# Kernel tuning notes

Measured on AMD Instinct MI355X. Metric: run time of the kernel, lower is better.

## Reference

```python
import jax, jax.numpy as jnp
import numpy as np
import math

B, H, W, CIN = 8, 64, 64, 192
INNER, K, N, P = 384, 2, 32, 64
NHK = INNER // P          # heads per scan direction = 6
NH = K * NHK              # total heads = 12
HID = 4 * CIN

def _silu(v):
    return v * jax.nn.sigmoid(v)

def setup_inputs() -> dict:
    key = jax.random.key(0)
    ks = jax.random.split(key, 12)
    x = jax.random.normal(ks[0], (B, H, W, CIN), jnp.float32)
    W_in = jax.random.normal(ks[1], (2 * INNER, CIN), jnp.float32) * 0.02
    conv_w = jax.random.normal(ks[2], (INNER, 1, 3, 3), jnp.float32) * 0.1
    conv_b = jnp.zeros((INNER,), jnp.float32)
    x_proj_weight = jax.random.normal(ks[3], (K, 2 * N + NHK, INNER), jnp.float32) * 0.02
    A_logs = jnp.log(jax.random.uniform(ks[4], (NH,), jnp.float32, 1.0, 16.0))
    Ds = jnp.ones((NH,), jnp.float32)
    u = jax.random.uniform(ks[5], (NH,), jnp.float32)
    dt = jnp.exp(u * (math.log(0.1) - math.log(0.001)) + math.log(0.001))
    dt = jnp.clip(dt, 1e-4, None)
    dt_bias = dt + jnp.log(-jnp.expm1(-dt))
    init_states = jnp.zeros((NH, P, N), jnp.float32)
    W_out = jax.random.normal(ks[6], (CIN, INNER), jnp.float32) * 0.02
    W1 = jax.random.normal(ks[7], (HID, CIN), jnp.float32) * 0.02
    b1 = jnp.zeros((HID,), jnp.float32)
    W2 = jax.random.normal(ks[8], (CIN, HID), jnp.float32) * 0.02
    b2 = jnp.zeros((CIN,), jnp.float32)
    return dict(x=x, W_in=W_in, conv_w=conv_w, conv_b=conv_b, x_proj_weight=x_proj_weight,
                A_logs=A_logs, Ds=Ds, dt_bias=dt_bias, init_states=init_states,
                W_out=W_out, W1=W1, b1=b1, W2=W2, b2=b2)

def reference(x, W_in, conv_w, conv_b, x_proj_weight, A_logs, Ds, dt_bias,
              init_states, W_out, W1, b1, W2, b2):
    Bb, Hh, Ww, Cin = x.shape
    L = Hh * Ww
    inner = W_in.shape[0] // 2
    shortcut = x
    # norm1 is identity (norm=None). in_proj (no bias), split into x and gate z
    xz = jnp.einsum('bhwc,dc->bhwd', x, W_in)
    xl, z = jnp.split(xz, 2, axis=-1)
    # depthwise conv (NCHW) + SiLU
    xc = jnp.transpose(xl, (0, 3, 1, 2))
    xc = jax.lax.conv_general_dilated(xc, conv_w, (1, 1), 'SAME',
                                      feature_group_count=inner,
                                      dimension_numbers=('NCHW', 'OIHW', 'NCHW'))
    xc = _silu(xc + conv_b[None, :, None, None])
    # cross scan: row-major and transposed (W-major) flattenings
    xs = jnp.stack([xc.reshape(Bb, inner, L),
                    jnp.transpose(xc, (0, 1, 3, 2)).reshape(Bb, inner, L)], axis=1)  # (B,K,inner,L)
    # project to B, C, dt per direction
    BCdt = jnp.einsum('bkdl,kcd->blkc', xs, x_proj_weight)  # (B,L,K,2N+NHK)
    Bs = BCdt[..., :N]                     # (B,L,K,N)
    Cs = BCdt[..., N:2 * N]                # (B,L,K,N)
    dt = BCdt[..., 2 * N:].reshape(Bb, L, NH)
    xh = jnp.transpose(xs, (0, 3, 1, 2)).reshape(Bb, L, NH, P)  # heads: k-major
    # Mamba2 selective scan (dt_softplus with bias)
    dt = jax.nn.softplus(dt + dt_bias)     # (B,L,NH)
    A = -jnp.exp(A_logs)                   # (NH,)
    da = jnp.exp(dt * A)                   # (B,L,NH)
    dtx = dt[..., None] * xh               # (B,L,NH,P)
    Bh = jnp.repeat(Bs, NHK, axis=2)       # (B,L,NH,N) group -> heads
    Ch = jnp.repeat(Cs, NHK, axis=2)
    h0 = jnp.broadcast_to(init_states, (Bb,) + init_states.shape)  # (B,NH,P,N)
    def step(h, inp):
        da_t, dtx_t, B_t, C_t = inp
        h = da_t[..., None, None] * h + dtx_t[..., None] * B_t[:, :, None, :]
        y_t = jnp.einsum('bhpn,bhn->bhp', h, C_t)
        return h, y_t
    _, ys = jax.lax.scan(step, h0, (jnp.moveaxis(da, 1, 0), jnp.moveaxis(dtx, 1, 0),
                                    jnp.moveaxis(Bh, 1, 0), jnp.moveaxis(Ch, 1, 0)))
    y = jnp.moveaxis(ys, 0, 1) + Ds[None, None, :, None] * xh  # (B,L,NH,P)
    out_y = jnp.transpose(y.reshape(Bb, L, K, inner), (0, 2, 3, 1))  # (B,K,inner,L)
    # scan_proj: undo each direction's flattening and sum
    y0 = out_y[:, 0].reshape(Bb, inner, Hh, Ww)
    y1 = jnp.transpose(out_y[:, 1].reshape(Bb, inner, Ww, Hh), (0, 1, 3, 2))
    yr = jnp.transpose((y0 + y1).reshape(Bb, inner, L), (0, 2, 1)).reshape(Bb, Hh, Ww, inner)
    # gate, out_proj, residual, MLP branch (dense is identity since in==out)
    yg = yr * _silu(z)
    out = shortcut + jnp.einsum('bhwd,cd->bhwc', yg, W_out)
    h1 = _silu(jnp.einsum('...c,dc->...d', out, W1) + b1)
    mlp = jnp.einsum('...d,cd->...c', h1, W2) + b2
    return out + mlp
```

## Files before the change

kernel.cpp:

```cpp
#include <hip/hip_runtime.h>
#include <math.h>

#define BB 8
#define HH 64
#define WW 64
#define CIN 192
#define INNER 384
#define LL 4096
#define NSTATE 32
#define PDIM 64
#define NHK 6
#define NHEADS 12
#define HID 768
#define CPROJ 70
#define QC 64
#define NC 64

#define WS_XLZ   0u
#define WS_XC    50331648u
#define WS_Y1    75497472u
#define WS_BCBF  100663296u
#define WS_DTRAW 109051904u
#define WS_DTV   119013376u
#define WS_CUMS  120586240u
#define WS_SHB   122159104u
#define WS_Y0    147324928u
#define WS_WINB  185073664u
#define WS_WPADB 185368576u
#define WS_WOUTB 185565184u
#define WS_W1B   185761792u
#define WS_W2B   186056704u
#define WS_REQ   186449920u

typedef __attribute__((ext_vector_type(8))) short short8;
typedef __attribute__((ext_vector_type(4))) float f32x4;

__device__ __forceinline__ float silu_f(float x) { return x / (1.f + __expf(-x)); }

__device__ __forceinline__ unsigned short f2bf(float f) {
    unsigned u = __float_as_uint(f);
    u += 0x7fffu + ((u >> 16) & 1u);
    return (unsigned short)(u >> 16);
}
__device__ __forceinline__ float bf2f(unsigned short u) {
    return __uint_as_float(((unsigned)u) << 16);
}

template<int AMODE>
__device__ __forceinline__ short8 load_a(const void* A, const unsigned short* Ay0,
                                         const unsigned short* Ay1, const unsigned short* Az,
                                         int row, int col, int Kd)
{
    if constexpr (AMODE == 0) {
        return *(const short8*)((const unsigned short*)A + (size_t)row * Kd + col);
    } else if constexpr (AMODE == 1) {
        const float* Af = (const float*)A + (size_t)row * Kd + col;
        const float4 v0 = *(const float4*)(Af);
        const float4 v1 = *(const float4*)(Af + 4);
        short8 r;
        r[0]=(short)f2bf(v0.x); r[1]=(short)f2bf(v0.y); r[2]=(short)f2bf(v0.z); r[3]=(short)f2bf(v0.w);
        r[4]=(short)f2bf(v1.x); r[5]=(short)f2bf(v1.y); r[6]=(short)f2bf(v1.z); r[7]=(short)f2bf(v1.w);
        return r;
    } else {
        const size_t yo = (size_t)row * INNER + col;
        const uint4 a  = *(const uint4*)(Ay0 + yo);
        const uint4 bv = *(const uint4*)(Ay1 + yo);
        const uint4 zv = *(const uint4*)(Az + (size_t)row * 768 + INNER + col);
        const unsigned ua[4]={a.x,a.y,a.z,a.w}, ub[4]={bv.x,bv.y,bv.z,bv.w}, uz[4]={zv.x,zv.y,zv.z,zv.w};
        short8 r;
        #pragma unroll
        for (int w2 = 0; w2 < 4; ++w2) {
            const float ylo = __uint_as_float(ua[w2] << 16) + __uint_as_float(ub[w2] << 16);
            const float yhi = __uint_as_float(ua[w2] & 0xffff0000u) + __uint_as_float(ub[w2] & 0xffff0000u);
            const float zlo = __uint_as_float(uz[w2] << 16);
            const float zhi = __uint_as_float(uz[w2] & 0xffff0000u);
            r[2*w2+0] = (short)f2bf(ylo * silu_f(zlo));
            r[2*w2+1] = (short)f2bf(yhi * silu_f(zhi));
        }
        return r;
    }
}

template<int EPI, int TRANSA, int AMODE>
__global__ __launch_bounds__(256)
void gemm_bf16(const void* __restrict__ A, const unsigned short* __restrict__ Wt,
               const float* __restrict__ bias, const float* __restrict__ res,
               float* __restrict__ Cf, unsigned short* __restrict__ Cb,
               const unsigned short* __restrict__ Ay0, const unsigned short* __restrict__ Ay1,
               const unsigned short* __restrict__ Az,
               int Kd, int ldc, int nmax)
{
    __shared__ __align__(16) short Als[128 * 64];
    __shared__ __align__(16) short Bls[128 * 64];
    const int tid = threadIdx.x;
    const int m0 = blockIdx.x * 128;
    const int n0 = blockIdx.y * 128;
    const int lane = tid & 63;
    const int wv = tid >> 6;
    const int wm = (wv >> 1) << 6;
    const int wn = (wv & 1) << 6;

    int am[4], ac[4];
    const unsigned short* gB[4];
    int lw[4];
    #pragma unroll
    for (int c = 0; c < 4; ++c) {
        const int idx = c * 256 + tid;
        const int row = idx >> 3;
        const int kb  = idx & 7;
        const int sb  = kb ^ (row & 7);
        lw[c] = row * 64 + sb * 8;
        int arow;
        const int mm = m0 + row;
        if (TRANSA) {
            const int bq = mm >> 12, lq = mm & 4095;
            arow = (bq << 12) + (((lq & 63) << 6) + (lq >> 6));
        } else {
            arow = mm;
        }
        am[c] = arow;
        ac[c] = kb * 8;
        gB[c] = Wt + (size_t)(n0 + row) * Kd + kb * 8;
    }

    f32x4 acc[4][4];
    #pragma unroll
    for (int i = 0; i < 4; ++i)
        #pragma unroll
        for (int j = 0; j < 4; ++j) acc[i][j] = (f32x4){0.f, 0.f, 0.f, 0.f};

    const int NT = Kd >> 6;
    short8 pA[4], pB[4];
    #pragma unroll
    for (int c = 0; c < 4; ++c) {
        pA[c] = load_a<AMODE>(A, Ay0, Ay1, Az, am[c], ac[c], Kd);
        pB[c] = *(const short8*)(gB[c]);
    }
    for (int kt = 0; kt < NT; ++kt) {
        __syncthreads();
        #pragma unroll
        for (int c = 0; c < 4; ++c) {
            *(short8*)&Als[lw[c]] = pA[c];
            *(short8*)&Bls[lw[c]] = pB[c];
        }
        __syncthreads();
        if (kt + 1 < NT) {
            #pragma unroll
            for (int c = 0; c < 4; ++c) {
                pA[c] = load_a<AMODE>(A, Ay0, Ay1, Az, am[c], ac[c] + (kt + 1) * 64, Kd);
                pB[c] = *(const short8*)(gB[c] + (kt + 1) * 64);
            }
        }
        #pragma unroll
        for (int ks = 0; ks < 2; ++ks) {
            short8 af[4], bfr[4];
            #pragma unroll
            for (int r = 0; r < 4; ++r) {
                const int rowa = wm + r * 16 + (lane & 15);
                const int rowb = wn + r * 16 + (lane & 15);
                const int kb = ks * 4 + (lane >> 4);
                af[r]  = *(const short8*)&Als[rowa * 64 + ((kb ^ (rowa & 7)) << 3)];
                bfr[r] = *(const short8*)&Bls[rowb * 64 + ((kb ^ (rowb & 7)) << 3)];
            }
            #pragma unroll
            for (int mr = 0; mr < 4; ++mr)
                #pragma unroll
                for (int nr = 0; nr < 4; ++nr)
                    acc[mr][nr] = __builtin_amdgcn_mfma_f32_16x16x32_bf16(af[mr], bfr[nr], acc[mr][nr], 0, 0, 0);
        }
    }
    #pragma unroll
    for (int mr = 0; mr < 4; ++mr) {
        #pragma unroll
        for (int nr = 0; nr < 4; ++nr) {
            const int n = n0 + wn + nr * 16 + (lane & 15);
            if (n >= nmax) continue;
            const int mb = m0 + wm + mr * 16 + ((lane >> 4) << 2);
            #pragma unroll
            for (int q = 0; q < 4; ++q) {
                const size_t off = (size_t)(mb + q) * ldc + n;
                float v = acc[mr][nr][q];
                if (EPI == 0) { Cf[off] = v; }
                else if (EPI == 1) { v = silu_f(v + bias[n]); Cb[off] = f2bf(v); }
                else if (EPI == 2) { v += bias[n] + res[off]; Cf[off] = v; }
                else if (EPI == 3) { v += res[off]; Cf[off] = v; Cb[off] = f2bf(v); }
                else if (EPI == 4) { Cb[off] = f2bf(v); }
                else if (EPI == 5) {
                    if (n < 64) Cb[(size_t)(mb + q) * 128 + n] = f2bf(v);
                    else        Cf[(size_t)(mb + q) * 12 + (n - 64)] = v;
                }
            }
        }
    }
}

__global__ __launch_bounds__(256)
void cvt_weights_kernel(const float* __restrict__ W_in, const float* __restrict__ W1,
                        const float* __restrict__ xpw, const float* __restrict__ W_out,
                        const float* __restrict__ W2,
                        unsigned short* __restrict__ Winb, unsigned short* __restrict__ W1b,
                        unsigned short* __restrict__ wpadb, unsigned short* __restrict__ Woutb,
                        unsigned short* __restrict__ W2b)
{
    int i = blockIdx.x * 256 + threadIdx.x;
    if (i < 147456) { Winb[i] = f2bf(W_in[i]); return; }
    i -= 147456;
    if (i < 147456) { W1b[i] = f2bf(W1[i]); return; }
    i -= 147456;
    if (i < 98304) {
        const int d = i % 384;
        const int rr = (i / 384) & 127;
        const int k = i / 49152;
        wpadb[i] = (rr < CPROJ) ? f2bf(xpw[((size_t)k * CPROJ + rr) * 384 + d]) : (unsigned short)0;
        return;
    }
    i -= 98304;
    if (i < 98304) {
        const int rr = i / 384;
        Woutb[i] = (rr < CIN) ? f2bf(W_out[i]) : (unsigned short)0;
        return;
    }
    i -= 98304;
    if (i < 196608) {
        const int rr = i / 768;
        W2b[i] = (rr < CIN) ? f2bf(W2[i]) : (unsigned short)0;
    }
}

__global__ __launch_bounds__(256)
void conv_dw_kernel(const unsigned short* __restrict__ xlz, const float* __restrict__ cw,
                    const float* __restrict__ cb, unsigned short* __restrict__ xcbf)
{
    const int t = blockIdx.x * 256 + threadIdx.x;
    const int dv = t % 48;
    int r = t / 48;
    const int j  = r & 63;  r >>= 6;
    const int ib = r & 7;   r >>= 3;
    const int b  = r;
    const int d0 = dv * 8;
    const int i0 = ib * 8;

    float wreg[72];
    {
        const float4* w4 = (const float4*)(cw + d0 * 9);
        #pragma unroll
        for (int u = 0; u < 18; ++u) {
            const float4 v = w4[u];
            wreg[4*u+0]=v.x; wreg[4*u+1]=v.y; wreg[4*u+2]=v.z; wreg[4*u+3]=v.w;
        }
    }
    float bias[8];
    {
        const float4 b0 = *(const float4*)(cb + d0);
        const float4 b1 = *(const float4*)(cb + d0 + 4);
        bias[0]=b0.x; bias[1]=b0.y; bias[2]=b0.z; bias[3]=b0.w;
        bias[4]=b1.x; bias[5]=b1.y; bias[6]=b1.z; bias[7]=b1.w;
    }

    const unsigned short* base = xlz + ((size_t)b << 12) * 768 + d0;
    const int jok[3] = { (j - 1 >= 0), 1, (j + 1 < WW) };

    unsigned rm[3][4], r0[3][4], rp[3][4];
    #pragma unroll
    for (int cj = 0; cj < 3; ++cj) {
        uint4 vm = make_uint4(0,0,0,0), v0 = make_uint4(0,0,0,0);
        if (jok[cj]) {
            if (i0 - 1 >= 0) vm = *(const uint4*)(base + (size_t)((i0-1) * 64 + j - 1 + cj) * 768);
            v0 = *(const uint4*)(base + (size_t)(i0 * 64 + j - 1 + cj) * 768);
        }
        rm[cj][0]=vm.x; rm[cj][1]=vm.y; rm[cj][2]=vm.z; rm[cj][3]=vm.w;
        r0[cj][0]=v0.x; r0[cj][1]=v0.y; r0[cj][2]=v0.z; r0[cj][3]=v0.w;
    }

    #pragma unroll
    for (int ii = 0; ii < 8; ++ii) {
        const int i = i0 + ii;
        #pragma unroll
        for (int cj = 0; cj < 3; ++cj) {
            uint4 vp = make_uint4(0,0,0,0);
            if (jok[cj] && (i + 1 < HH))
                vp = *(const uint4*)(base + (size_t)((i+1) * 64 + j - 1 + cj) * 768);
            rp[cj][0]=vp.x; rp[cj][1]=vp.y; rp[cj][2]=vp.z; rp[cj][3]=vp.w;
        }
        float acc[8];
        #pragma unroll
        for (int ch = 0; ch < 8; ++ch) acc[ch] = bias[ch];
        #pragma unroll
        for (int cj = 0; cj < 3; ++cj) {
            #pragma unroll
            for (int w2 = 0; w2 < 4; ++w2) {
                acc[2*w2+0] = fmaf(__uint_as_float(rm[cj][w2] << 16),        wreg[(2*w2+0)*9 + cj],     acc[2*w2+0]);
                acc[2*w2+1] = fmaf(__uint_as_float(rm[cj][w2] & 0xffff0000u), wreg[(2*w2+1)*9 + cj],     acc[2*w2+1]);
                acc[2*w2+0] = fmaf(__uint_as_float(r0[cj][w2] << 16),        wreg[(2*w2+0)*9 + 3 + cj], acc[2*w2+0]);
                acc[2*w2+1] = fmaf(__uint_as_float(r0[cj][w2] & 0xffff0000u), wreg[(2*w2+1)*9 + 3 + cj], acc[2*w2+1]);
                acc[2*w2+0] = fmaf(__uint_as_float(rp[cj][w2] << 16),        wreg[(2*w2+0)*9 + 6 + cj], acc[2*w2+0]);
                acc[2*w2+1] = fmaf(__uint_as_float(rp[cj][w2] & 0xffff0000u), wreg[(2*w2+1)*9 + 6 + cj], acc[2*w2+1]);
            }
        }
        unsigned o[4];
        #pragma unroll
        for (int w2 = 0; w2 < 4; ++w2) {
            const unsigned lo = f2bf(silu_f(acc[2*w2+0]));
            const unsigned hi = f2bf(silu_f(acc[2*w2+1]));
            o[w2] = lo | (hi << 16);
        }
        *(uint4*)(xcbf + ((size_t)(b << 12) + (size_t)(i * 64 + j)) * INNER + d0) =
            make_uint4(o[0], o[1], o[2], o[3]);
        #pragma unroll
        for (int cj = 0; cj < 3; ++cj)
            #pragma unroll
            for (int w2 = 0; w2 < 4; ++w2) {
                rm[cj][w2] = r0[cj][w2];
                r0[cj][w2] = rp[cj][w2];
            }
    }
}

__global__ __launch_bounds__(256)
void dtcums_kernel(const float* __restrict__ dtraw, const float* __restrict__ dt_bias,
                   const float* __restrict__ A_logs,
                   float* __restrict__ dtv, float* __restrict__ cums)
{
    const int w = blockIdx.x * 4 + (threadIdx.x >> 6);
    const int lane = threadIdx.x & 63;
    const int b = w / (NHEADS * NC);
    const int rem = w - b * (NHEADS * NC);
    const int h = rem / NC;
    const int c = rem - h * NC;
    const int k = h / NHK;
    const int hq = h - k * NHK;
    const int l = c * QC + lane;
    const float dtr = dtraw[(((size_t)b * LL + l) * 2 + k) * 6 + hq];
    const float xx = dtr + dt_bias[h];
    const float sp = (xx > 20.f) ? xx : log1pf(expf(xx));
    float s = -expf(A_logs[h]) * sp;
    #pragma unroll
    for (int d = 1; d < 64; d <<= 1) {
        const float o = __shfl_up(s, d);
        if (lane >= d) s += o;
    }
    dtv[((size_t)b * LL + l) * NHEADS + h] = sp;
    cums[((size_t)b * LL + l) * NHEADS + h] = s;
}

__global__ __launch_bounds__(256)
void chunk_state_kernel(const unsigned short* __restrict__ xcbf, const unsigned short* __restrict__ BCbf,
                        const float* __restrict__ dtv, const float* __restrict__ cums,
                        unsigned short* __restrict__ SHb)
{
    __shared__ __align__(16) unsigned short Xb[PDIM][72];
    __shared__ __align__(16) unsigned short Bsc[NSTATE][72];
    __shared__ float cuS[QC], rs[QC];
    const int c = blockIdx.x, h = blockIdx.y, b = blockIdx.z;
    const int k = h / NHK;
    const int dch0 = (h - k * NHK) * PDIM;
    const int tid = threadIdx.x;
    const int lane = tid & 63;
    const int w = tid >> 6;

    #pragma unroll
    for (int r2 = 0; r2 < 2; ++r2) {
        const int idx = tid + r2 * 256;
        const int m = idx >> 3, pg = idx & 7;
        const int pos = (k == 0) ? (c * QC + m) : (m * QC + c);
        const uint4 v = *(const uint4*)(xcbf + (((size_t)b << 12) + pos) * INNER + dch0 + pg * 8);
        const unsigned ua[4] = {v.x, v.y, v.z, v.w};
        #pragma unroll
        for (int e2 = 0; e2 < 4; ++e2) {
            Xb[pg * 8 + 2*e2 + 0][m] = (unsigned short)(ua[e2] & 0xffffu);
            Xb[pg * 8 + 2*e2 + 1][m] = (unsigned short)(ua[e2] >> 16);
        }
    }
    if (tid < QC)
        cuS[tid] = cums[((size_t)b * LL + c * QC + tid) * NHEADS + h];
    __syncthreads();
    if (tid < QC)
        rs[tid] = dtv[((size_t)b * LL + c * QC + tid) * NHEADS + h] * __expf(cuS[QC-1] - cuS[tid]);
    __syncthreads();
    #pragma unroll
    for (int r = 0; r < 8; ++r) {
        const int idx = tid + r * 256;
        const int m = idx >> 5, n = idx & 31;
        Bsc[n][m] = f2bf(rs[m] * bf2f(BCbf[(((size_t)b * LL + c * QC + m) * 2 + k) * 64 + n]));
    }
    __syncthreads();

    const int rowf = lane & 15;
    const int ko   = lane >> 4;
    f32x4 acc[2] = {{0.f,0.f,0.f,0.f},{0.f,0.f,0.f,0.f}};
    #pragma unroll
    for (int ks = 0; ks < 2; ++ks) {
        const short8 af = *(const short8*)&Xb[w * 16 + rowf][ks * 32 + ko * 8];
        #pragma unroll
        for (int nt = 0; nt < 2; ++nt) {
            const short8 bfr = *(const short8*)&Bsc[nt * 16 + rowf][ks * 32 + ko * 8];
            acc[nt] = __builtin_amdgcn_mfma_f32_16x16x32_bf16(af, bfr, acc[nt], 0, 0, 0);
        }
    }
    unsigned short* base = SHb + ((((size_t)b * NHEADS + h) * NC + c) * PDIM) * NSTATE;
    #pragma unroll
    for (int nt = 0; nt < 2; ++nt) {
        #pragma unroll
        for (int q = 0; q < 4; ++q) {
            const int p = w * 16 + ko * 4 + q;
            base[p * NSTATE + nt * 16 + rowf] = f2bf(acc[nt][q]);
        }
    }
}

__global__ __launch_bounds__(64)
void state_scan_kernel(unsigned short* __restrict__ SHb, const float* __restrict__ cums,
                       const float* __restrict__ init_states)
{
    __shared__ float decays[NC];
    const int g = blockIdx.x;
    const int bh = g >> 2;
    const int quarter = g & 3;
    const int b = bh / NHEADS;
    const int h = bh % NHEADS;
    const int tid = threadIdx.x;
    decays[tid] = __expf(cums[((size_t)b * LL + tid * QC + QC - 1) * NHEADS + h]);
    __syncthreads();
    const int p = quarter * 16 + (tid >> 2);
    const int nb = (tid & 3) * 8;
    float hs[8];
    {
        const float* is = init_states + ((size_t)h * PDIM + p) * NSTATE + nb;
        #pragma unroll
        for (int i = 0; i < 8; ++i) hs[i] = is[i];
    }
    unsigned short* base = SHb + (((size_t)b * NHEADS + h) * NC) * (PDIM * NSTATE) + p * NSTATE + nb;
    for (int c = 0; c < NC; ++c) {
        unsigned short* slot = base + (size_t)c * (PDIM * NSTATE);
        const uint4 sv = *(const uint4*)slot;
        const unsigned ua[4] = {sv.x, sv.y, sv.z, sv.w};
        unsigned o[4];
        #pragma unroll
        for (int w2 = 0; w2 < 4; ++w2)
            o[w2] = (unsigned)f2bf(hs[2*w2]) | ((unsigned)f2bf(hs[2*w2+1]) << 16);
        *(uint4*)slot = make_uint4(o[0], o[1], o[2], o[3]);
        const float dc = decays[c];
        #pragma unroll
        for (int w2 = 0; w2 < 4; ++w2) {
            hs[2*w2+0] = fmaf(dc, hs[2*w2+0], __uint_as_float(ua[w2] << 16));
            hs[2*w2+1] = fmaf(dc, hs[2*w2+1], __uint_as_float(ua[w2] & 0xffff0000u));
        }
    }
}

__global__ __launch_bounds__(256)
void intra_kernel(const unsigned short* __restrict__ xcbf, const unsigned short* __restrict__ BCbf,
                  const float* __restrict__ dtv, const float* __restrict__ cums,
                  const unsigned short* __restrict__ SHb, const float* __restrict__ Ds,
                  unsigned short* __restrict__ y0, unsigned short* __restrict__ y1)
{
    __shared__ __align__(16) unsigned short Bs[QC][40];
    __shared__ __align__(16) unsigned short Cs[QC][40];
    __shared__ __align__(16) unsigned short Hs[PDIM][40];
    __shared__ __align__(16) unsigned short Xb[PDIM][72];
    __shared__ __align__(16) unsigned short Gb[QC][72];
    __shared__ float cuS[QC], dtS[QC], Ei[QC];
    const int c = blockIdx.x, h = blockIdx.y, b = blockIdx.z;
    const int k = h / NHK;
    const int dch0 = (h - k * NHK) * PDIM;
    const int tid = threadIdx.x;
    const int lane = tid & 63;
    const int w = tid >> 6;

    #pragma unroll
    for (int r2 = 0; r2 < 2; ++r2) {
        const int idx = tid + r2 * 256;
        const int m = idx >> 3, pg = idx & 7;
        const int pos = (k == 0) ? (c * QC + m) : (m * QC + c);
        const uint4 v = *(const uint4*)(xcbf + (((size_t)b << 12) + pos) * INNER + dch0 + pg * 8);
        const unsigned ua[4] = {v.x, v.y, v.z, v.w};
        #pragma unroll
        for (int e2 = 0; e2 < 4; ++e2) {
            Xb[pg * 8 + 2*e2 + 0][m] = (unsigned short)(ua[e2] & 0xffffu);
            Xb[pg * 8 + 2*e2 + 1][m] = (unsigned short)(ua[e2] >> 16);
        }
    }
    #pragma unroll
    for (int r = 0; r < 2; ++r) {
        const int idx = tid + r * 256;
        const int i = idx >> 3, ch = idx & 7;
        const uint4 v = *(const uint4*)(BCbf + (((size_t)b * LL + c * QC + i) * 2 + k) * 64 + ch * 8);
        if (ch < 4) *(uint4*)&Bs[i][ch * 8] = v;
        else        *(uint4*)&Cs[i][(ch - 4) * 8] = v;
    }
    {
        const int p = tid >> 2, ch = tid & 3;
        *(uint4*)&Hs[p][ch * 8] =
            *(const uint4*)(SHb + ((((size_t)b * NHEADS + h) * NC + c) * PDIM + p) * NSTATE + ch * 8);
    }
    if (tid < QC) {
        const size_t o = ((size_t)b * LL + c * QC + tid) * NHEADS + h;
        const float cu = cums[o];
        cuS[tid] = cu;
        dtS[tid] = dtv[o];
        Ei[tid]  = __expf(cu);
    }
    __syncthreads();

    const int rowf = lane & 15;
    const int ko   = lane >> 4;
    const short8 cfrag = *(const short8*)&Cs[w * 16 + rowf][ko * 8];

    f32x4 graw[4];
    #pragma unroll
    for (int mt = 0; mt < 4; ++mt) {
        const short8 bfrag = *(const short8*)&Bs[mt * 16 + rowf][ko * 8];
        graw[mt] = __builtin_amdgcn_mfma_f32_16x16x32_bf16(cfrag, bfrag, (f32x4){0.f,0.f,0.f,0.f}, 0, 0, 0);
    }
    #pragma unroll
    for (int mt = 0; mt < 4; ++mt) {
        const int m = mt * 16 + rowf;
        const float cum = cuS[m];
        const float dtm = dtS[m];
        #pragma unroll
        for (int q = 0; q < 4; ++q) {
            const int i = w * 16 + ko * 4 + q;
            float g = 0.f;
            if (m <= i) g = __expf(fminf(cuS[i] - cum, 0.f)) * dtm * graw[mt][q];
            Gb[i][m] = f2bf(g);
        }
    }
    f32x4 acc[4];
    #pragma unroll
    for (int pt = 0; pt < 4; ++pt) {
        const short8 hfrag = *(const short8*)&Hs[pt * 16 + rowf][ko * 8];
        acc[pt] = __builtin_amdgcn_mfma_f32_16x16x32_bf16(cfrag, hfrag, (f32x4){0.f,0.f,0.f,0.f}, 0, 0, 0);
    }
    const float Dh = Ds[h];
    #pragma unroll
    for (int pt = 0; pt < 4; ++pt) {
        const int p = pt * 16 + rowf;
        #pragma unroll
        for (int q = 0; q < 4; ++q) {
            const int i = w * 16 + ko * 4 + q;
            acc[pt][q] = acc[pt][q] * Ei[i] + Dh * bf2f(Xb[p][i]);
        }
    }
    #pragma unroll
    for (int ks = 0; ks < 2; ++ks) {
        const short8 gfrag = *(const short8*)&Gb[w * 16 + rowf][ks * 32 + ko * 8];
        #pragma unroll
        for (int pt = 0; pt < 4; ++pt) {
            const short8 xfrag = *(const short8*)&Xb[pt * 16 + rowf][ks * 32 + ko * 8];
            acc[pt] = __builtin_amdgcn_mfma_f32_16x16x32_bf16(gfrag, xfrag, acc[pt], 0, 0, 0);
        }
    }
    unsigned short* yk = (k == 0) ? y0 : y1;
    #pragma unroll
    for (int pt = 0; pt < 4; ++pt) {
        const int p = pt * 16 + rowf;
        #pragma unroll
        for (int q = 0; q < 4; ++q) {
            const int i = w * 16 + ko * 4 + q;
            const int pos = (k == 0) ? (c * QC + i) : (i * QC + c);
            yk[(((size_t)b << 12) + pos) * INNER + dch0 + p] = f2bf(acc[pt][q]);
        }
    }
}

__global__ __launch_bounds__(256)
void report_ws_kernel(float* __restrict__ out, int n, float val)
{
    const int e = blockIdx.x * 256 + threadIdx.x;
    if (e < n) out[e] = val;
}

extern "C" void kernel_launch(void* const* d_in, const int* in_sizes, int n_in,
                              void* d_out, int out_size, void* d_ws, size_t ws_size,
                              hipStream_t stream)
{
    const float* x          = (const float*)d_in[0];
    const float* W_in       = (const float*)d_in[1];
    const float* conv_w     = (const float*)d_in[2];
    const float* conv_b     = (const float*)d_in[3];
    const float* xpw        = (const float*)d_in[4];
    const float* A_logs     = (const float*)d_in[5];
    const float* Ds         = (const float*)d_in[6];
    const float* dt_bias    = (const float*)d_in[7];
    const float* init_states= (const float*)d_in[8];
    const float* W_out      = (const float*)d_in[9];
    const float* W1         = (const float*)d_in[10];
    const float* b1         = (const float*)d_in[11];
    const float* W2         = (const float*)d_in[12];
    const float* b2         = (const float*)d_in[13];
    float* out = (float*)d_out;

    if (ws_size < (size_t)WS_REQ) {
        const float mib = (float)((double)ws_size / 1048576.0);
        report_ws_kernel<<<(out_size + 255) / 256, 256, 0, stream>>>(out, out_size, mib);
        return;
    }

    char* ws = (char*)d_ws;
    unsigned short* xlz   = (unsigned short*)(ws + WS_XLZ);
    unsigned short* xc_bf = (unsigned short*)(ws + WS_XC);
    unsigned short* y1    = (unsigned short*)(ws + WS_Y1);
    unsigned short* BCbf  = (unsigned short*)(ws + WS_BCBF);
    float* dtraw = (float*)(ws + WS_DTRAW);
    float* dtv   = (float*)(ws + WS_DTV);
    float* cums  = (float*)(ws + WS_CUMS);
    unsigned short* SHb   = (unsigned short*)(ws + WS_SHB);
    unsigned short* y0    = (unsigned short*)(ws + WS_Y0);
    unsigned short* Winb  = (unsigned short*)(ws + WS_WINB);
    unsigned short* wpadb = (unsigned short*)(ws + WS_WPADB);
    unsigned short* Woutb = (unsigned short*)(ws + WS_WOUTB);
    unsigned short* W1b   = (unsigned short*)(ws + WS_W1B);
    unsigned short* W2b   = (unsigned short*)(ws + WS_W2B);
    unsigned short* out_bf = (unsigned short*)(ws + WS_BCBF);
    unsigned short* h1_bf  = (unsigned short*)(ws + WS_XLZ);

    const int M = BB * LL;

    cvt_weights_kernel<<<(688128 + 255) / 256, 256, 0, stream>>>(W_in, W1, xpw, W_out, W2,
                                                                 Winb, W1b, wpadb, Woutb, W2b);

    gemm_bf16<4,0,1><<<dim3(M/128, HID/128), 256, 0, stream>>>(x, Winb, nullptr, nullptr, nullptr, xlz,
                                                               nullptr, nullptr, nullptr, CIN, HID, HID);

    conv_dw_kernel<<<196608 / 256, 256, 0, stream>>>(xlz, conv_w, conv_b, xc_bf);

    gemm_bf16<5,0,0><<<dim3(M/128, 1), 256, 0, stream>>>(xc_bf, wpadb, nullptr, nullptr, dtraw, BCbf,
                                                         nullptr, nullptr, nullptr, INNER, 0, CPROJ);
    gemm_bf16<5,1,0><<<dim3(M/128, 1), 256, 0, stream>>>(xc_bf, wpadb + 128 * INNER, nullptr, nullptr, dtraw + 6, BCbf + 64,
                                                         nullptr, nullptr, nullptr, INNER, 0, CPROJ);

    dtcums_kernel<<<(BB * NHEADS * NC) / 4, 256, 0, stream>>>(dtraw, dt_bias, A_logs, dtv, cums);

    chunk_state_kernel<<<dim3(NC, NHEADS, BB), 256, 0, stream>>>(xc_bf, BCbf, dtv, cums, SHb);
    state_scan_kernel<<<BB * NHEADS * 4, 64, 0, stream>>>(SHb, cums, init_states);
    intra_kernel<<<dim3(NC, NHEADS, BB), 256, 0, stream>>>(xc_bf, BCbf, dtv, cums, SHb, Ds, y0, y1);

    gemm_bf16<3,0,2><<<dim3(M/128, 2), 256, 0, stream>>>(nullptr, Woutb, nullptr, x, out, out_bf,
                                                         y0, y1, xlz, INNER, CIN, CIN);

    gemm_bf16<1,0,0><<<dim3(M/128, HID/128), 256, 0, stream>>>(out_bf, W1b, b1, nullptr, nullptr, h1_bf,
                                                               nullptr, nullptr, nullptr, CIN, HID, HID);
    gemm_bf16<2,0,0><<<dim3(M/128, 2), 256, 0, stream>>>(h1_bf, W2b, b2, out, out, nullptr,
                                                         nullptr, nullptr, nullptr, HID, CIN, CIN);
}
```

Baseline: 244.5 us.

## Keep full-K A tile resident in LDS and loop over all N tiles per block

Adds a GEMM kernel for the K=192, N=768 projections (in_proj and MLP W1). Each block loads its whole 128x192 A slab into LDS once, then walks all six 128-wide N tiles while streaming weight tiles through a register-prefetched B buffer. This replaces a 2D grid where each block reloaded, and for in_proj reconverted, its A rows for every N tile. The cost is a grid six times smaller (256 blocks), heavier LDS use per block, and no pipelining across the epilogue stores.

```diff
diff --git a/kernel.cpp b/kernel.cpp
--- a/kernel.cpp
+++ b/kernel.cpp
@@ -194,6 +194,107 @@
     }
 }
 
+template<int EPI, int AMODE>
+__global__ __launch_bounds__(256)
+void gemm_nloop(const void* __restrict__ A, const unsigned short* __restrict__ Wt,
+                const float* __restrict__ bias, unsigned short* __restrict__ Cb)
+{
+    __shared__ __align__(16) unsigned short Als[128 * 192];
+    __shared__ __align__(16) unsigned short Bls[128 * 64];
+    const int tid = threadIdx.x;
+    const int m0 = blockIdx.x * 128;
+    const int lane = tid & 63;
+    const int wv = tid >> 6;
+    const int wm = (wv >> 1) << 6;
+    const int wn = (wv & 1) << 6;
+    const int Kd = 192;
+
+    #pragma unroll
+    for (int c = 0; c < 12; ++c) {
+        const int idx = c * 256 + tid;
+        const int row = idx / 24;
+        const int kb  = idx - row * 24;
+        const int sb  = (kb & ~7) | ((kb & 7) ^ (row & 7));
+        const short8 v = load_a<AMODE>(A, nullptr, nullptr, nullptr, m0 + row, kb * 8, Kd);
+        *(short8*)&Als[row * 192 + sb * 8] = v;
+    }
+
+    int wrow[4], wkb[4], lw[4];
+    #pragma unroll
+    for (int c = 0; c < 4; ++c) {
+        const int idx = c * 256 + tid;
+        const int row = idx >> 3;
+        const int kb  = idx & 7;
+        wrow[c] = row;
+        wkb[c]  = kb;
+        lw[c]   = row * 64 + (kb ^ (row & 7)) * 8;
+    }
+
+    f32x4 acc[4][4];
+    short8 pB[4];
+    #pragma unroll
+    for (int c = 0; c < 4; ++c)
+        pB[c] = *(const short8*)(Wt + (size_t)wrow[c] * Kd + wkb[c] * 8);
+
+    for (int s = 0; s < 18; ++s) {
+        const int nt = s / 3;
+        const int kt = s - nt * 3;
+        if (kt == 0) {
+            #pragma unroll
+            for (int i = 0; i < 4; ++i)
+                #pragma unroll
+                for (int j = 0; j < 4; ++j) acc[i][j] = (f32x4){0.f, 0.f, 0.f, 0.f};
+        }
+        __syncthreads();
+        #pragma unroll
+        for (int c = 0; c < 4; ++c)
+            *(short8*)&Bls[lw[c]] = pB[c];
+        __syncthreads();
+        if (s + 1 < 18) {
+            const int nt2 = (s + 1) / 3;
+            const int kt2 = (s + 1) - nt2 * 3;
+            #pragma unroll
+            for (int c = 0; c < 4; ++c)
+                pB[c] = *(const short8*)(Wt + (size_t)(nt2 * 128 + wrow[c]) * Kd + kt2 * 64 + wkb[c] * 8);
+        }
+        #pragma unroll
+        for (int ks = 0; ks < 2; ++ks) {
+            short8 af[4], bfr[4];
+            #pragma unroll
+            for (int r = 0; r < 4; ++r) {
+                const int rowa = wm + r * 16 + (lane & 15);
+                const int rowb = wn + r * 16 + (lane & 15);
+                const int kbf = kt * 8 + ks * 4 + (lane >> 4);
+                const int sba = (kbf & ~7) | ((kbf & 7) ^ (rowa & 7));
+                af[r]  = *(const short8*)&Als[rowa * 192 + sba * 8];
+                const int kb2 = ks * 4 + (lane >> 4);
+                bfr[r] = *(const short8*)&Bls[rowb * 64 + ((kb2 ^ (rowb & 7)) << 3)];
+            }
+            #pragma unroll
+            for (int mr = 0; mr < 4; ++mr)
+                #pragma unroll
+                for (int nr = 0; nr < 4; ++nr)
+                    acc[mr][nr] = __builtin_amdgcn_mfma_f32_16x16x32_bf16(af[mr], bfr[nr], acc[mr][nr], 0, 0, 0);
+        }
+        if (kt == 2) {
+            #pragma unroll
+            for (int mr = 0; mr < 4; ++mr) {
+                #pragma unroll
+                for (int nr = 0; nr < 4; ++nr) {
+                    const int n = nt * 128 + wn + nr * 16 + (lane & 15);
+                    const int mb = m0 + wm + mr * 16 + ((lane >> 4) << 2);
+                    #pragma unroll
+                    for (int q = 0; q < 4; ++q) {
+                        float v = acc[mr][nr][q];
+                        if (EPI == 1) v = silu_f(v + bias[n]);
+                        Cb[(size_t)(mb + q) * HID + n] = f2bf(v);
+                    }
+                }
+            }
+        }
+    }
+}
+
 __global__ __launch_bounds__(256)
 void cvt_weights_kernel(const float* __restrict__ W_in, const float* __restrict__ W1,
                         const float* __restrict__ xpw, const float* __restrict__ W_out,
@@ -619,8 +720,7 @@
     cvt_weights_kernel<<<(688128 + 255) / 256, 256, 0, stream>>>(W_in, W1, xpw, W_out, W2,
                                                                  Winb, W1b, wpadb, Woutb, W2b);
 
-    gemm_bf16<4,0,1><<<dim3(M/128, HID/128), 256, 0, stream>>>(x, Winb, nullptr, nullptr, nullptr, xlz,
-                                                               nullptr, nullptr, nullptr, CIN, HID, HID);
+    gemm_nloop<4,1><<<M/128, 256, 0, stream>>>(x, Winb, nullptr, xlz);
 
     conv_dw_kernel<<<196608 / 256, 256, 0, stream>>>(xlz, conv_w, conv_b, xc_bf);
 
@@ -638,8 +738,8 @@
     gemm_bf16<3,0,2><<<dim3(M/128, 2), 256, 0, stream>>>(nullptr, Woutb, nullptr, x, out, out_bf,
                                                          y0, y1, xlz, INNER, CIN, CIN);
 
-    gemm_bf16<1,0,0><<<dim3(M/128, HID/128), 256, 0, stream>>>(out_bf, W1b, b1, nullptr, nullptr, h1_bf,
-                                                               nullptr, nullptr, nullptr, CIN, HID, HID);
+    gemm_nloop<1,0><<<M/128, 256, 0, stream>>>(out_bf, W1b, b1, h1_bf);
+
     gemm_bf16<2,0,0><<<dim3(M/128, 2), 256, 0, stream>>>(h1_bf, W2b, b2, out, out, nullptr,
                                                          nullptr, nullptr, nullptr, HID, CIN, CIN);
 }
```

Measured after the change: 251.0 us. +2.6%, slower.
